# Performance work log

Hardware: AMD Instinct MI355X
Metric: run time of the kernel (lower is better)

Reference implementation:

```python
import jax, jax.numpy as jnp
import numpy as np

BATCH, T, D_MODEL, D_STATE = 32, 4096, 256, 256
RMIN, RMAX, MAX_PHASE = 0.9, 0.999, 6.283
NEG_SLOPE = 0.01  # F.leaky_relu default


def setup_inputs() -> dict:
    key = jax.random.key(0)
    ks = jax.random.split(key, 12)
    x = jax.random.normal(ks[0], (BATCH, T, D_MODEL), jnp.float32)
    done = jnp.zeros((BATCH, T), jnp.bool_)
    h0_re = jnp.zeros((BATCH, D_STATE), jnp.float32)
    h0_im = jnp.zeros((BATCH, D_STATE), jnp.float32)
    # LRU eigenvalue init: |lambda| ~ U[rmin, rmax] (Orvieto et al.)
    u1 = jax.random.uniform(ks[1], (D_STATE,), jnp.float32)
    u2 = jax.random.uniform(ks[2], (D_STATE,), jnp.float32)
    nu_log = jnp.log(-0.5 * jnp.log(u1 * (RMAX**2 - RMIN**2) + RMIN**2))
    theta_log = jnp.log(MAX_PHASE * u2)
    lam_abs = jnp.exp(-jnp.exp(nu_log))
    gamma_log = jnp.log(jnp.sqrt(1.0 - lam_abs**2))
    sB = 1.0 / np.sqrt(2.0 * D_MODEL)
    sC = 1.0 / np.sqrt(D_STATE)
    B_re = jax.random.normal(ks[3], (D_STATE, D_MODEL), jnp.float32) * sB
    B_im = jax.random.normal(ks[4], (D_STATE, D_MODEL), jnp.float32) * sB
    C_re = jax.random.normal(ks[5], (D_STATE, D_STATE), jnp.float32) * sC
    C_im = jax.random.normal(ks[6], (D_STATE, D_STATE), jnp.float32) * sC
    D_mat = jax.random.normal(ks[7], (D_STATE, D_MODEL), jnp.float32) * (1.0 / np.sqrt(D_MODEL))
    mlp_w = jax.random.normal(ks[8], (D_MODEL, D_STATE), jnp.float32) * (1.0 / np.sqrt(D_STATE))
    mlp_b = jnp.zeros((D_MODEL,), jnp.float32)
    ln1_g = jnp.ones((D_MODEL,), jnp.float32); ln1_b = jnp.zeros((D_MODEL,), jnp.float32)
    ln2_g = jnp.ones((D_STATE,), jnp.float32); ln2_b = jnp.zeros((D_STATE,), jnp.float32)
    ln3_g = jnp.ones((D_MODEL,), jnp.float32); ln3_b = jnp.zeros((D_MODEL,), jnp.float32)
    return dict(x=x, done=done, h0_re=h0_re, h0_im=h0_im, nu_log=nu_log,
                theta_log=theta_log, gamma_log=gamma_log, B_re=B_re, B_im=B_im,
                C_re=C_re, C_im=C_im, D_mat=D_mat, mlp_w=mlp_w, mlp_b=mlp_b,
                ln1_g=ln1_g, ln1_b=ln1_b, ln2_g=ln2_g, ln2_b=ln2_b,
                ln3_g=ln3_g, ln3_b=ln3_b)


def _layernorm(x, g, b, eps=1e-5):
    mu = jnp.mean(x, axis=-1, keepdims=True)
    var = jnp.var(x, axis=-1, keepdims=True)
    return (x - mu) * jax.lax.rsqrt(var + eps) * g + b


def _leaky(x):
    return jnp.where(x >= 0, x, NEG_SLOPE * x)


def _forward(x, done, h0_re, h0_im, nu_log, theta_log, gamma_log, B_re, B_im,
             C_re, C_im, D_mat, mlp_w, mlp_b, ln1_g, ln1_b, ln2_g, ln2_b,
             ln3_g, ln3_b):
    z = _layernorm(x, ln1_g, ln1_b)          # [B,T,D]
    skip = z
    z = _leaky(z)
    # diagonal complex recurrence params
    lam_abs = jnp.exp(-jnp.exp(nu_log))
    theta = jnp.exp(theta_log)
    lam_re = lam_abs * jnp.cos(theta)        # [N]
    lam_im = lam_abs * jnp.sin(theta)
    gamma = jnp.exp(gamma_log)
    # input projection: gamma * (B z_t), complex
    u_re = jnp.einsum('btd,nd->btn', z, B_re) * gamma
    u_im = jnp.einsum('btd,nd->btn', z, B_im) * gamma
    mask = 1.0 - done.astype(z.dtype)        # [B,T], reset state where done

    def step(carry, inp):
        hr, hi = carry
        ur, ui, m = inp                       # [B,N],[B,N],[B]
        hr = hr * m[:, None]
        hi = hi * m[:, None]
        nr = lam_re * hr - lam_im * hi + ur
        ni = lam_re * hi + lam_im * hr + ui
        return (nr, ni), (nr, ni)

    xs = (jnp.swapaxes(u_re, 0, 1), jnp.swapaxes(u_im, 0, 1), jnp.swapaxes(mask, 0, 1))
    (_, _), (hs_re, hs_im) = jax.lax.scan(step, (h0_re, h0_im), xs)
    hs_re = jnp.swapaxes(hs_re, 0, 1)         # [B,T,N]
    hs_im = jnp.swapaxes(hs_im, 0, 1)
    # y = Re(C h) + D z
    y = (jnp.einsum('btn,mn->btm', hs_re, C_re)
         - jnp.einsum('btn,mn->btm', hs_im, C_im)
         + jnp.einsum('btd,nd->btn', z, D_mat))
    y = _leaky(_layernorm(y, ln2_g, ln2_b))
    y = jnp.einsum('btn,dn->btd', y, mlp_w) + mlp_b
    y = _layernorm(y, ln3_g, ln3_b)
    return y + skip


def reference(x, done, h0_re, h0_im, nu_log, theta_log, gamma_log, B_re, B_im,
              C_re, C_im, D_mat, mlp_w, mlp_b, ln1_g, ln1_b, ln2_g, ln2_b,
              ln3_g, ln3_b):
    return _forward(x, done, h0_re, h0_im, nu_log, theta_log, gamma_log,
                    B_re, B_im, C_re, C_im, D_mat, mlp_w, mlp_b,
                    ln1_g, ln1_b, ln2_g, ln2_b, ln3_g, ln3_b)
```

## Files before the change

### kernel.cpp

```cpp
#include <hip/hip_runtime.h>

#define BATCH 32
#define TLEN  4096
#define DM    256
#define NS    256
#define BT    (BATCH*TLEN)
#define CHL   64
#define NCH   (TLEN/CHL)

typedef unsigned short u16;
typedef __bf16 bf16x8 __attribute__((ext_vector_type(8)));
typedef float  f32x4  __attribute__((ext_vector_type(4)));

__device__ __forceinline__ u16 f2bf(float f) {
  unsigned u = __builtin_bit_cast(unsigned, f);
  u += 0x7FFFu + ((u >> 16) & 1u);
  return (u16)(u >> 16);
}
__device__ __forceinline__ float bf2f(u16 h) {
  unsigned u = ((unsigned)h) << 16;
  return __builtin_bit_cast(float, u);
}
__device__ __forceinline__ float wsum(float v) {
  #pragma unroll
  for (int m = 32; m >= 1; m >>= 1) v += __shfl_xor(v, m, 64);
  return v;
}
__device__ __forceinline__ void gload_lds16(const void* g, void* l) {
  __builtin_amdgcn_global_load_lds(
      (const __attribute__((address_space(1))) void*)(uintptr_t)g,
      (__attribute__((address_space(3))) void*)(unsigned)(uintptr_t)l,
      16, 0, 0);
}
#define VMCNT(N)  asm volatile("s_waitcnt vmcnt(" #N ")" ::: "memory")
#define LGKM0()   asm volatile("s_waitcnt lgkmcnt(0)" ::: "memory")
#define BARRIER() do { __builtin_amdgcn_s_barrier(); asm volatile("" ::: "memory"); } while (0)

__global__ void k_prep(const float* __restrict__ nu_log, const float* __restrict__ th_log,
                       const float* __restrict__ ga_log,
                       const float* __restrict__ B_re, const float* __restrict__ B_im,
                       const float* __restrict__ C_re, const float* __restrict__ C_im,
                       const float* __restrict__ D_mat, const float* __restrict__ mlp_w,
                       float* __restrict__ lam_re, float* __restrict__ lam_im,
                       u16* __restrict__ WB, u16* __restrict__ W2, u16* __restrict__ WM)
{
  const int tid = blockIdx.x * blockDim.x + threadIdx.x;
  const int nt  = gridDim.x * blockDim.x;
  for (int i = tid; i < NS; i += nt) {
    float la = expf(-expf(nu_log[i]));
    float th = expf(th_log[i]);
    lam_re[i] = la * cosf(th);
    lam_im[i] = la * sinf(th);
  }
  for (int i = tid; i < 512 * DM; i += nt) {
    int n = i >> 8, d = i & 255;
    float v = (n < 256) ? B_re[n * DM + d] * expf(ga_log[n])
                        : B_im[(n - 256) * DM + d] * expf(ga_log[n - 256]);
    WB[i] = f2bf(v);
  }
  for (int i = tid; i < 256 * 768; i += nt) {
    int n = i / 768, k = i - n * 768;
    float v;
    if (k < 256)      v =  C_re[n * 256 + k];
    else if (k < 512) v = -C_im[n * 256 + (k - 256)];
    else              v =  D_mat[n * 256 + (k - 512)];
    W2[i] = f2bf(v);
  }
  for (int i = tid; i < 256 * 256; i += nt) WM[i] = f2bf(mlp_w[i]);
}

__global__ __launch_bounds__(256) void k_ln1(const float* __restrict__ x,
                                             const float* __restrict__ g, const float* __restrict__ b,
                                             u16* __restrict__ za)
{
  const size_t row = (size_t)blockIdx.x * 4 + (threadIdx.x >> 6);
  const int lane = threadIdx.x & 63;
  float4 v = ((const float4*)(x + row * DM))[lane];
  float s = wsum(v.x + v.y + v.z + v.w);
  float q = wsum(v.x * v.x + v.y * v.y + v.z * v.z + v.w * v.w);
  float mean = s * (1.f / DM);
  float rstd = rsqrtf(q * (1.f / DM) - mean * mean + 1e-5f);
  float4 gg = ((const float4*)g)[lane];
  float4 bb = ((const float4*)b)[lane];
  float z0 = (v.x - mean) * rstd * gg.x + bb.x;
  float z1 = (v.y - mean) * rstd * gg.y + bb.y;
  float z2 = (v.z - mean) * rstd * gg.z + bb.z;
  float z3 = (v.w - mean) * rstd * gg.w + bb.w;
  ushort4 zl;
  zl.x = f2bf(z0 >= 0.f ? z0 : 0.01f * z0);
  zl.y = f2bf(z1 >= 0.f ? z1 : 0.01f * z1);
  zl.z = f2bf(z2 >= 0.f ? z2 : 0.01f * z2);
  zl.w = f2bf(z3 >= 0.f ? z3 : 0.01f * z3);
  ((ushort4*)(za + row * DM))[lane] = zl;
}

template <int EPI>
__global__ __launch_bounds__(512, 2) void gemm_fused(
    const u16* __restrict__ A0, int lda0, int ksplit,
    const u16* __restrict__ A1, int lda1,
    int K, const u16* __restrict__ W, int ldw,
    const float* __restrict__ g, const float* __restrict__ b,
    const float* __restrict__ bias, const u16* __restrict__ zsrc,
    u16* __restrict__ outb, float* __restrict__ outf, int ldo)
{
  __shared__ __align__(16) u16 As[2][256 * 64];
  __shared__ __align__(16) u16 Bs[2][256 * 64];
  int mt, nw0;
  if constexpr (EPI == 0) {
    const int bid = blockIdx.x;
    const int xcd = bid & 7, s = bid >> 3;
    mt  = xcd * 64 + (s >> 1);
    nw0 = (s & 1) << 8;
  } else { mt = blockIdx.x; nw0 = 0; }
  const int m0 = mt * 256;
  const int tid = threadIdx.x;
  const int w = tid >> 6, lane = tid & 63;
  const int wr = w >> 1, wc = w & 1;

  f32x4 acc[4][8] = {};

  auto STAGE_A = [&](int p, int k0, int half) {
    const bool second = (k0 >= ksplit);
    const u16* Asrc = second ? A1 : A0;
    const int  alda = second ? lda1 : lda0;
    const int  ak   = second ? (k0 - ksplit) : k0;
    #pragma unroll
    for (int j = 0; j < 2; ++j) {
      const int r = half * 16 + w * 2 + j;
      const int row = r * 8 + (lane >> 3);
      const int col = (((lane & 7) ^ (row & 7)) << 3);
      gload_lds16(Asrc + (size_t)(m0 + row) * alda + ak + col, &As[p][r * 512]);
    }
  };
  auto STAGE_B = [&](int p, int k0, int half) {
    #pragma unroll
    for (int j = 0; j < 2; ++j) {
      const int r = half * 16 + w * 2 + j;
      const int row = r * 8 + (lane >> 3);
      const int col = (((lane & 7) ^ (row & 7)) << 3);
      gload_lds16(W + (size_t)(nw0 + row) * ldw + k0 + col, &Bs[p][r * 512]);
    }
  };

  const int NT = K >> 6;
  STAGE_A(0, 0, 0); STAGE_A(0, 0, 1);
  STAGE_B(0, 0, 0); STAGE_B(0, 0, 1);
  if (NT > 1) { STAGE_A(1, 64, 0); STAGE_A(1, 64, 1); VMCNT(4); }
  else        { VMCNT(0); }
  BARRIER();

  const int lq = (lane >> 4) << 3;

  for (int t = 0; t < NT; ++t) {
    const int p = t & 1;
    const int pn = p ^ 1;
    bf16x8 af[4][2];
    bf16x8 bfr[2][2];

    #pragma unroll
    for (int mi = 0; mi < 4; ++mi) {
      const int ra = wr * 64 + mi * 16 + (lane & 15);
      #pragma unroll
      for (int kki = 0; kki < 2; ++kki) {
        const int koff = kki * 32 + lq;
        af[mi][kki] = *(const bf16x8*)((const char*)&As[p][0] + ra * 128 + ((koff * 2) ^ ((ra & 7) << 4)));
      }
    }
    #pragma unroll
    for (int nn = 0; nn < 2; ++nn) {
      const int rb = wc * 128 + nn * 16 + (lane & 15);
      #pragma unroll
      for (int kki = 0; kki < 2; ++kki) {
        const int koff = kki * 32 + lq;
        bfr[nn][kki] = *(const bf16x8*)((const char*)&Bs[p][0] + rb * 128 + ((koff * 2) ^ ((rb & 7) << 4)));
      }
    }
    if (t + 1 < NT) STAGE_B(pn, (t + 1) << 6, 0);
    BARRIER(); LGKM0();
    __builtin_amdgcn_s_setprio(1);
    #pragma unroll
    for (int kki = 0; kki < 2; ++kki)
      #pragma unroll
      for (int nn = 0; nn < 2; ++nn)
        #pragma unroll
        for (int mi = 0; mi < 4; ++mi)
          acc[mi][nn] = __builtin_amdgcn_mfma_f32_16x16x32_bf16(af[mi][kki], bfr[nn][kki], acc[mi][nn], 0, 0, 0);
    __builtin_amdgcn_s_setprio(0);
    BARRIER();

    #pragma unroll
    for (int q = 1; q < 4; ++q) {
      #pragma unroll
      for (int nn = 0; nn < 2; ++nn) {
        const int rb = wc * 128 + (q * 2 + nn) * 16 + (lane & 15);
        #pragma unroll
        for (int kki = 0; kki < 2; ++kki) {
          const int koff = kki * 32 + lq;
          bfr[nn][kki] = *(const bf16x8*)((const char*)&Bs[p][0] + rb * 128 + ((koff * 2) ^ ((rb & 7) << 4)));
        }
      }
      if (q == 1)      { if (t + 1 < NT) STAGE_B(pn, (t + 1) << 6, 1); }
      else if (q == 2) { if (t + 2 < NT) STAGE_A(p,  (t + 2) << 6, 0); }
      else             { if (t + 2 < NT) STAGE_A(p,  (t + 2) << 6, 1); }
      BARRIER(); LGKM0();
      __builtin_amdgcn_s_setprio(1);
      #pragma unroll
      for (int kki = 0; kki < 2; ++kki)
        #pragma unroll
        for (int nn = 0; nn < 2; ++nn)
          #pragma unroll
          for (int mi = 0; mi < 4; ++mi)
            acc[mi][q * 2 + nn] = __builtin_amdgcn_mfma_f32_16x16x32_bf16(af[mi][kki], bfr[nn][kki], acc[mi][q * 2 + nn], 0, 0, 0);
      __builtin_amdgcn_s_setprio(0);
      if (q == 3) { if (t + 2 < NT) { VMCNT(4); } else { VMCNT(0); } }
      BARRIER();
    }
  }

  const int rq = (lane >> 4) << 2;

  if constexpr (EPI == 0) {
    #pragma unroll
    for (int mi = 0; mi < 4; ++mi) {
      #pragma unroll
      for (int rr = 0; rr < 4; ++rr) {
        const int row = wr * 64 + mi * 16 + rq + rr;
        const size_t rbase = (size_t)(m0 + row) * ldo + nw0;
        #pragma unroll
        for (int ni = 0; ni < 8; ++ni) {
          const int col = wc * 128 + ni * 16 + (lane & 15);
          outb[rbase + col] = f2bf(acc[mi][ni][rr]);
        }
      }
    }
    return;
  }

  float g8[8], b8[8], bias8[8];
  #pragma unroll
  for (int ni = 0; ni < 8; ++ni) {
    const int col = wc * 128 + ni * 16 + (lane & 15);
    g8[ni] = g[col]; b8[ni] = b[col];
    if constexpr (EPI == 2) bias8[ni] = bias[col];
  }

  float* red = (float*)&As[0][0];
  #pragma unroll
  for (int mi = 0; mi < 4; ++mi) {
    #pragma unroll
    for (int rr = 0; rr < 4; ++rr) {
      float s = 0.f, q = 0.f;
      #pragma unroll
      for (int ni = 0; ni < 8; ++ni) {
        float v = acc[mi][ni][rr];
        if constexpr (EPI == 2) v += bias8[ni];
        s += v; q += v * v;
      }
      #pragma unroll
      for (int mm = 1; mm < 16; mm <<= 1) {
        s += __shfl_xor(s, mm, 64);
        q += __shfl_xor(q, mm, 64);
      }
      if ((lane & 15) == 0) {
        const int row = wr * 64 + mi * 16 + rq + rr;
        red[row * 4 + wc * 2]     = s;
        red[row * 4 + wc * 2 + 1] = q;
      }
    }
  }
  __syncthreads();

  #pragma unroll
  for (int mi = 0; mi < 4; ++mi) {
    #pragma unroll
    for (int rr = 0; rr < 4; ++rr) {
      const int row = wr * 64 + mi * 16 + rq + rr;
      const float S = red[row * 4] + red[row * 4 + 2];
      const float Q = red[row * 4 + 1] + red[row * 4 + 3];
      const float mean = S * (1.f / 256.f);
      const float rstd = rsqrtf(Q * (1.f / 256.f) - mean * mean + 1e-5f);
      const size_t rbase = (size_t)(m0 + row) * 256;
      #pragma unroll
      for (int ni = 0; ni < 8; ++ni) {
        const int col = wc * 128 + ni * 16 + (lane & 15);
        float v = acc[mi][ni][rr];
        if constexpr (EPI == 2) v += bias8[ni];
        float t = (v - mean) * rstd * g8[ni] + b8[ni];
        if constexpr (EPI == 1) {
          t = t >= 0.f ? t : 0.01f * t;
          outb[rbase + col] = f2bf(t);
        } else {
          float zv = bf2f(zsrc[rbase + col]);
          zv = zv >= 0.f ? zv : 100.f * zv;
          outf[rbase + col] = t + zv;
        }
      }
    }
  }
}

__global__ __launch_bounds__(256) void scan_passA(const u16* __restrict__ u,
    const unsigned char* __restrict__ done,
    const float* __restrict__ lam_re, const float* __restrict__ lam_im,
    float* __restrict__ Ere, float* __restrict__ Eim,
    float* __restrict__ Are, float* __restrict__ Aim)
{
  const int b = blockIdx.x / NCH, c = blockIdx.x % NCH;
  const int n = threadIdx.x;
  const float lr = lam_re[n], li = lam_im[n];
  float hre = 0.f, him = 0.f, pm = 1.f;
  const int t0 = c * CHL;
  for (int t = t0; t < t0 + CHL; ++t) {
    const float m = done[b * TLEN + t] ? 0.f : 1.f;
    pm *= m;
    const float hr = hre * m, hi = him * m;
    const size_t base = ((size_t)(b * TLEN + t)) * 512;
    const float ur = bf2f(u[base + n]), ui = bf2f(u[base + 256 + n]);
    hre = lr * hr - li * hi + ur;
    him = lr * hi + li * hr + ui;
  }
  const size_t idx = ((size_t)(b * NCH + c)) * NS + n;
  Ere[idx] = hre; Eim[idx] = him;
  float pr = lr, pi = li;
  #pragma unroll
  for (int s = 0; s < 6; ++s) { float a = pr * pr - pi * pi; float bq = 2.f * pr * pi; pr = a; pi = bq; }
  Are[idx] = pr * pm; Aim[idx] = pi * pm;
}

__global__ __launch_bounds__(256) void scan_comb(const float* __restrict__ h0re,
    const float* __restrict__ h0im,
    const float* __restrict__ Are, const float* __restrict__ Aim,
    const float* __restrict__ Ere, const float* __restrict__ Eim,
    float* __restrict__ Sre, float* __restrict__ Sim)
{
  const int b = blockIdx.x, n = threadIdx.x;
  float sre = h0re[b * NS + n], sim = h0im[b * NS + n];
  for (int c = 0; c < NCH; ++c) {
    const size_t idx = ((size_t)(b * NCH + c)) * NS + n;
    Sre[idx] = sre; Sim[idx] = sim;
    const float ar = Are[idx], ai = Aim[idx];
    const float nr = ar * sre - ai * sim + Ere[idx];
    const float ni = ar * sim + ai * sre + Eim[idx];
    sre = nr; sim = ni;
  }
}

__global__ __launch_bounds__(256) void scan_passC(u16* __restrict__ u,
    const unsigned char* __restrict__ done,
    const float* __restrict__ lam_re, const float* __restrict__ lam_im,
    const float* __restrict__ Sre, const float* __restrict__ Sim)
{
  const int b = blockIdx.x / NCH, c = blockIdx.x % NCH;
  const int n = threadIdx.x;
  const float lr = lam_re[n], li = lam_im[n];
  const size_t sidx = ((size_t)(b * NCH + c)) * NS + n;
  float hre = Sre[sidx], him = Sim[sidx];
  const int t0 = c * CHL;
  for (int t = t0; t < t0 + CHL; ++t) {
    const float m = done[b * TLEN + t] ? 0.f : 1.f;
    const float hr = hre * m, hi = him * m;
    const size_t base = ((size_t)(b * TLEN + t)) * 512;
    const float ur = bf2f(u[base + n]), ui = bf2f(u[base + 256 + n]);
    hre = lr * hr - li * hi + ur;
    him = lr * hi + li * hr + ui;
    u[base + n]       = f2bf(hre);
    u[base + 256 + n] = f2bf(him);
  }
}

extern "C" void kernel_launch(void* const* d_in, const int* in_sizes, int n_in,
                              void* d_out, int out_size, void* d_ws, size_t ws_size,
                              hipStream_t stream)
{
  const float* x      = (const float*)d_in[0];
  const unsigned char* done = (const unsigned char*)d_in[1];
  const float* h0re   = (const float*)d_in[2];
  const float* h0im   = (const float*)d_in[3];
  const float* nu_log = (const float*)d_in[4];
  const float* th_log = (const float*)d_in[5];
  const float* ga_log = (const float*)d_in[6];
  const float* B_re   = (const float*)d_in[7];
  const float* B_im   = (const float*)d_in[8];
  const float* C_re   = (const float*)d_in[9];
  const float* C_im   = (const float*)d_in[10];
  const float* D_mat  = (const float*)d_in[11];
  const float* mlp_w  = (const float*)d_in[12];
  const float* mlp_b  = (const float*)d_in[13];
  const float* ln1_g  = (const float*)d_in[14];
  const float* ln1_b  = (const float*)d_in[15];
  const float* ln2_g  = (const float*)d_in[16];
  const float* ln2_b  = (const float*)d_in[17];
  const float* ln3_g  = (const float*)d_in[18];
  const float* ln3_b  = (const float*)d_in[19];
  (void)in_sizes; (void)n_in; (void)out_size; (void)ws_size;

  char* ws = (char*)d_ws;
  float* lam_re = (float*)(ws + 0);
  float* lam_im = (float*)(ws + 1024);
  u16* WB = (u16*)(ws + 4096);
  u16* W2 = (u16*)(ws + 4096 + 512 * 256 * 2);
  u16* WM = (u16*)(ws + 4096 + 512 * 256 * 2 + 256 * 768 * 2);

  size_t off = (size_t)1 << 20;
  u16* za    = (u16*)(ws + off); off += (size_t)BT * DM * 2;
  u16* ubuf  = (u16*)(ws + off); off += (size_t)BT * 512 * 2;
  u16* ybuf  = (u16*)(ws + off); off += (size_t)BT * NS * 2;
  float* Ere = (float*)(ws + off); off += (size_t)BATCH * NCH * NS * 4;
  float* Eim = (float*)(ws + off); off += (size_t)BATCH * NCH * NS * 4;
  float* Are = (float*)(ws + off); off += (size_t)BATCH * NCH * NS * 4;
  float* Aim = (float*)(ws + off); off += (size_t)BATCH * NCH * NS * 4;
  float* Sre = (float*)(ws + off); off += (size_t)BATCH * NCH * NS * 4;
  float* Sim = (float*)(ws + off); off += (size_t)BATCH * NCH * NS * 4;

  k_prep<<<256, 256, 0, stream>>>(nu_log, th_log, ga_log, B_re, B_im, C_re, C_im,
                                  D_mat, mlp_w, lam_re, lam_im, WB, W2, WM);
  k_ln1<<<BT / 4, 256, 0, stream>>>(x, ln1_g, ln1_b, za);
  gemm_fused<0><<<1024, 512, 0, stream>>>(za, 256, 1 << 28, nullptr, 0,
                                          256, WB, 256, nullptr, nullptr,
                                          nullptr, nullptr, ubuf, nullptr, 512);
  scan_passA<<<BATCH * NCH, 256, 0, stream>>>(ubuf, done, lam_re, lam_im, Ere, Eim, Are, Aim);
  scan_comb <<<BATCH,       256, 0, stream>>>(h0re, h0im, Are, Aim, Ere, Eim, Sre, Sim);
  scan_passC<<<BATCH * NCH, 256, 0, stream>>>(ubuf, done, lam_re, lam_im, Sre, Sim);
  gemm_fused<1><<<BT / 256, 512, 0, stream>>>(ubuf, 512, 512, za, 256,
                                              768, W2, 768, ln2_g, ln2_b,
                                              nullptr, nullptr, ybuf, nullptr, 256);
  gemm_fused<2><<<BT / 256, 512, 0, stream>>>(ybuf, 256, 256, ybuf, 256,
                                              256, WM, 256, ln3_g, ln3_b,
                                              mlp_b, za, nullptr, (float*)d_out, 256);
}
```

Measured before the change: 330.5 us.

## Fuse chunk-local scan summary into input-projection GEMM epilogue

Drops the separate scan_passA kernel. The first GEMM epilogue now computes, for each 64-step chunk, the complex decay product and the end state straight from the accumulator registers, using a warp shuffle scan across the row quads. Real and imaginary parts come from separate column halves, so each half writes its own partial E and scan_comb adds the two. This removes one full read of the 256 MB u buffer and one launch, at the cost of a heavier GEMM epilogue and higher register pressure.

New measurement: 367.9 us. 11.3% more time.

```diff
diff --git a/kernel.cpp b/kernel.cpp
--- a/kernel.cpp
+++ b/kernel.cpp
@@ -7,6 +7,7 @@
 #define BT    (BATCH*TLEN)
 #define CHL   64
 #define NCH   (TLEN/CHL)
+#define PSTRIDE ((size_t)BATCH*NCH*NS)
 
 typedef unsigned short u16;
 typedef __bf16 bf16x8 __attribute__((ext_vector_type(8)));
@@ -101,7 +102,11 @@
     int K, const u16* __restrict__ W, int ldw,
     const float* __restrict__ g, const float* __restrict__ b,
     const float* __restrict__ bias, const u16* __restrict__ zsrc,
-    u16* __restrict__ outb, float* __restrict__ outf, int ldo)
+    u16* __restrict__ outb, float* __restrict__ outf, int ldo,
+    const unsigned char* __restrict__ done,
+    const float* __restrict__ lamr, const float* __restrict__ lami,
+    float* __restrict__ Ebase_r, float* __restrict__ Ebase_i,
+    float* __restrict__ Apr, float* __restrict__ Api)
 {
   __shared__ __align__(16) u16 As[2][256 * 64];
   __shared__ __align__(16) u16 Bs[2][256 * 64];
@@ -233,6 +238,64 @@
         }
       }
     }
+    const int hq = lane >> 4;
+    const int ln = lane & 15;
+    const int gchunk = (m0 >> 6) + wr;
+    const int trow0 = m0 + wr * 64;
+    const int part = nw0 >> 8;
+    uchar4 dn[4];
+    #pragma unroll
+    for (int mi = 0; mi < 4; ++mi)
+      dn[mi] = *(const uchar4*)(done + trow0 + mi * 16 + hq * 4);
+    #pragma unroll
+    for (int ni = 0; ni < 8; ++ni) {
+      const int n = wc * 128 + ni * 16 + ln;
+      const float lr = lamr[n], li = lami[n];
+      float Ar = 1.f, Ai = 0.f, Er = 0.f, Ei = 0.f;
+      #pragma unroll
+      for (int mi = 0; mi < 4; ++mi) {
+        float ar = 1.f, ai = 0.f, er = 0.f, ei = 0.f;
+        #pragma unroll
+        for (int rr = 0; rr < 4; ++rr) {
+          const unsigned char db = (rr == 0) ? dn[mi].x : (rr == 1) ? dn[mi].y
+                                 : (rr == 2) ? dn[mi].z : dn[mi].w;
+          const float m = db ? 0.f : 1.f;
+          const float uv = acc[mi][ni][rr];
+          const float ur = part == 0 ? uv : 0.f;
+          const float ui = part == 0 ? 0.f : uv;
+          const float lmr = lr * m, lmi = li * m;
+          const float na_r = lmr * ar - lmi * ai, na_i = lmr * ai + lmi * ar;
+          ar = na_r; ai = na_i;
+          const float ne_r = lmr * er - lmi * ei + ur;
+          const float ne_i = lmr * ei + lmi * er + ui;
+          er = ne_r; ei = ne_i;
+        }
+        #pragma unroll
+        for (int d = 1; d <= 2; d <<= 1) {
+          int sl = lane - 16 * d; sl = sl < 0 ? lane : sl;
+          const float pa_r = __shfl(ar, sl, 64), pa_i = __shfl(ai, sl, 64);
+          const float pe_r = __shfl(er, sl, 64), pe_i = __shfl(ei, sl, 64);
+          if (hq >= d) {
+            const float ca_r = ar * pa_r - ai * pa_i, ca_i = ar * pa_i + ai * pa_r;
+            const float ce_r = er + (ar * pe_r - ai * pe_i);
+            const float ce_i = ei + (ar * pe_i + ai * pe_r);
+            ar = ca_r; ai = ca_i; er = ce_r; ei = ce_i;
+          }
+        }
+        ar = __shfl(ar, ln + 48, 64); ai = __shfl(ai, ln + 48, 64);
+        er = __shfl(er, ln + 48, 64); ei = __shfl(ei, ln + 48, 64);
+        const float nA_r = ar * Ar - ai * Ai, nA_i = ar * Ai + ai * Ar;
+        const float nE_r = er + (ar * Er - ai * Ei);
+        const float nE_i = ei + (ar * Ei + ai * Er);
+        Ar = nA_r; Ai = nA_i; Er = nE_r; Ei = nE_i;
+      }
+      if (hq == 0) {
+        const size_t idx = (size_t)gchunk * 256 + n;
+        Ebase_r[(size_t)part * PSTRIDE + idx] = Er;
+        Ebase_i[(size_t)part * PSTRIDE + idx] = Ei;
+        if (part == 0) { Apr[idx] = Ar; Api[idx] = Ai; }
+      }
+    }
     return;
   }
 
@@ -299,38 +362,10 @@
   }
 }
 
-__global__ __launch_bounds__(256) void scan_passA(const u16* __restrict__ u,
-    const unsigned char* __restrict__ done,
-    const float* __restrict__ lam_re, const float* __restrict__ lam_im,
-    float* __restrict__ Ere, float* __restrict__ Eim,
-    float* __restrict__ Are, float* __restrict__ Aim)
-{
-  const int b = blockIdx.x / NCH, c = blockIdx.x % NCH;
-  const int n = threadIdx.x;
-  const float lr = lam_re[n], li = lam_im[n];
-  float hre = 0.f, him = 0.f, pm = 1.f;
-  const int t0 = c * CHL;
-  for (int t = t0; t < t0 + CHL; ++t) {
-    const float m = done[b * TLEN + t] ? 0.f : 1.f;
-    pm *= m;
-    const float hr = hre * m, hi = him * m;
-    const size_t base = ((size_t)(b * TLEN + t)) * 512;
-    const float ur = bf2f(u[base + n]), ui = bf2f(u[base + 256 + n]);
-    hre = lr * hr - li * hi + ur;
-    him = lr * hi + li * hr + ui;
-  }
-  const size_t idx = ((size_t)(b * NCH + c)) * NS + n;
-  Ere[idx] = hre; Eim[idx] = him;
-  float pr = lr, pi = li;
-  #pragma unroll
-  for (int s = 0; s < 6; ++s) { float a = pr * pr - pi * pi; float bq = 2.f * pr * pi; pr = a; pi = bq; }
-  Are[idx] = pr * pm; Aim[idx] = pi * pm;
-}
-
 __global__ __launch_bounds__(256) void scan_comb(const float* __restrict__ h0re,
     const float* __restrict__ h0im,
-    const float* __restrict__ Are, const float* __restrict__ Aim,
-    const float* __restrict__ Ere, const float* __restrict__ Eim,
+    const float* __restrict__ Apr, const float* __restrict__ Api,
+    const float* __restrict__ Er, const float* __restrict__ Ei,
     float* __restrict__ Sre, float* __restrict__ Sim)
 {
   const int b = blockIdx.x, n = threadIdx.x;
@@ -338,9 +373,11 @@
   for (int c = 0; c < NCH; ++c) {
     const size_t idx = ((size_t)(b * NCH + c)) * NS + n;
     Sre[idx] = sre; Sim[idx] = sim;
-    const float ar = Are[idx], ai = Aim[idx];
-    const float nr = ar * sre - ai * sim + Ere[idx];
-    const float ni = ar * sim + ai * sre + Eim[idx];
+    const float ar = Apr[idx], ai = Api[idx];
+    const float er = Er[idx] + Er[PSTRIDE + idx];
+    const float ei = Ei[idx] + Ei[PSTRIDE + idx];
+    const float nr = ar * sre - ai * sim + er;
+    const float ni = ar * sim + ai * sre + ei;
     sre = nr; sim = ni;
   }
 }
@@ -405,26 +442,30 @@
   u16* za    = (u16*)(ws + off); off += (size_t)BT * DM * 2;
   u16* ubuf  = (u16*)(ws + off); off += (size_t)BT * 512 * 2;
   u16* ybuf  = (u16*)(ws + off); off += (size_t)BT * NS * 2;
-  float* Ere = (float*)(ws + off); off += (size_t)BATCH * NCH * NS * 4;
-  float* Eim = (float*)(ws + off); off += (size_t)BATCH * NCH * NS * 4;
-  float* Are = (float*)(ws + off); off += (size_t)BATCH * NCH * NS * 4;
-  float* Aim = (float*)(ws + off); off += (size_t)BATCH * NCH * NS * 4;
-  float* Sre = (float*)(ws + off); off += (size_t)BATCH * NCH * NS * 4;
-  float* Sim = (float*)(ws + off); off += (size_t)BATCH * NCH * NS * 4;
+  float* Apr = (float*)(ws + off); off += PSTRIDE * 4;
+  float* Api = (float*)(ws + off); off += PSTRIDE * 4;
+  float* Er  = (float*)(ws + off); off += PSTRIDE * 4 * 2;
+  float* Ei  = (float*)(ws + off); off += PSTRIDE * 4 * 2;
+  float* Sre = (float*)(ws + off); off += PSTRIDE * 4;
+  float* Sim = (float*)(ws + off); off += PSTRIDE * 4;
 
   k_prep<<<256, 256, 0, stream>>>(nu_log, th_log, ga_log, B_re, B_im, C_re, C_im,
                                   D_mat, mlp_w, lam_re, lam_im, WB, W2, WM);
   k_ln1<<<BT / 4, 256, 0, stream>>>(x, ln1_g, ln1_b, za);
   gemm_fused<0><<<1024, 512, 0, stream>>>(za, 256, 1 << 28, nullptr, 0,
                                           256, WB, 256, nullptr, nullptr,
-                                          nullptr, nullptr, ubuf, nullptr, 512);
-  scan_passA<<<BATCH * NCH, 256, 0, stream>>>(ubuf, done, lam_re, lam_im, Ere, Eim, Are, Aim);
-  scan_comb <<<BATCH,       256, 0, stream>>>(h0re, h0im, Are, Aim, Ere, Eim, Sre, Sim);
+                                          nullptr, nullptr, ubuf, nullptr, 512,
+                                          done, lam_re, lam_im, Er, Ei, Apr, Api);
+  scan_comb<<<BATCH, 256, 0, stream>>>(h0re, h0im, Apr, Api, Er, Ei, Sre, Sim);
   scan_passC<<<BATCH * NCH, 256, 0, stream>>>(ubuf, done, lam_re, lam_im, Sre, Sim);
   gemm_fused<1><<<BT / 256, 512, 0, stream>>>(ubuf, 512, 512, za, 256,
                                               768, W2, 768, ln2_g, ln2_b,
-                                              nullptr, nullptr, ybuf, nullptr, 256);
+                                              nullptr, nullptr, ybuf, nullptr, 256,
+                                              nullptr, nullptr, nullptr,
+                                              nullptr, nullptr, nullptr, nullptr);
   gemm_fused<2><<<BT / 256, 512, 0, stream>>>(ybuf, 256, 256, ybuf, 256,
                                               256, WM, 256, ln3_g, ln3_b,
-                                              mlp_b, za, nullptr, (float*)d_out, 256);
-}
+                                              mlp_b, za, nullptr, (float*)d_out, 256,
+                                              nullptr, nullptr, nullptr,
+                                              nullptr, nullptr, nullptr, nullptr);
+}
```

## Split GEMM kernel into specialized u-projection and smaller-tile LayerNorm GEMMs

Applied to the files above, without the earlier changes.

The templated GEMM is split in two. One kernel keeps the 256x256 tile for the input projection, with its strides and trip count hard-coded. The two LayerNorm-epilogue GEMMs use a new kernel with 128-row M tiles, K steps of 32, a new LDS swizzle and launch bounds raised to 4 blocks per CU. This doubles the grid (1024 blocks) so occupancy and latency hiding improve. In exchange, the full 256-column B tile is reloaded twice as often per output row and there are more barriers per K.

Measured after the change: 346.0 us. +4.7%, slower.

```diff
diff --git a/kernel.cpp b/kernel.cpp
--- a/kernel.cpp
+++ b/kernel.cpp
@@ -94,24 +94,16 @@
   ((ushort4*)(za + row * DM))[lane] = zl;
 }
 
-template <int EPI>
-__global__ __launch_bounds__(512, 2) void gemm_fused(
-    const u16* __restrict__ A0, int lda0, int ksplit,
-    const u16* __restrict__ A1, int lda1,
-    int K, const u16* __restrict__ W, int ldw,
-    const float* __restrict__ g, const float* __restrict__ b,
-    const float* __restrict__ bias, const u16* __restrict__ zsrc,
-    u16* __restrict__ outb, float* __restrict__ outf, int ldo)
+__global__ __launch_bounds__(512, 2) void gemm_u4(
+    const u16* __restrict__ A0, const u16* __restrict__ W,
+    u16* __restrict__ outb)
 {
   __shared__ __align__(16) u16 As[2][256 * 64];
   __shared__ __align__(16) u16 Bs[2][256 * 64];
-  int mt, nw0;
-  if constexpr (EPI == 0) {
-    const int bid = blockIdx.x;
-    const int xcd = bid & 7, s = bid >> 3;
-    mt  = xcd * 64 + (s >> 1);
-    nw0 = (s & 1) << 8;
-  } else { mt = blockIdx.x; nw0 = 0; }
+  const int bid = blockIdx.x;
+  const int xcd = bid & 7, sl = bid >> 3;
+  const int mt  = xcd * 64 + (sl >> 1);
+  const int nw0 = (sl & 1) << 8;
   const int m0 = mt * 256;
   const int tid = threadIdx.x;
   const int w = tid >> 6, lane = tid & 63;
@@ -120,16 +112,12 @@
   f32x4 acc[4][8] = {};
 
   auto STAGE_A = [&](int p, int k0, int half) {
-    const bool second = (k0 >= ksplit);
-    const u16* Asrc = second ? A1 : A0;
-    const int  alda = second ? lda1 : lda0;
-    const int  ak   = second ? (k0 - ksplit) : k0;
     #pragma unroll
     for (int j = 0; j < 2; ++j) {
       const int r = half * 16 + w * 2 + j;
       const int row = r * 8 + (lane >> 3);
       const int col = (((lane & 7) ^ (row & 7)) << 3);
-      gload_lds16(Asrc + (size_t)(m0 + row) * alda + ak + col, &As[p][r * 512]);
+      gload_lds16(A0 + (size_t)(m0 + row) * 256 + k0 + col, &As[p][r * 512]);
     }
   };
   auto STAGE_B = [&](int p, int k0, int half) {
@@ -138,15 +126,14 @@
       const int r = half * 16 + w * 2 + j;
       const int row = r * 8 + (lane >> 3);
       const int col = (((lane & 7) ^ (row & 7)) << 3);
-      gload_lds16(W + (size_t)(nw0 + row) * ldw + k0 + col, &Bs[p][r * 512]);
+      gload_lds16(W + (size_t)(nw0 + row) * 256 + k0 + col, &Bs[p][r * 512]);
     }
   };
 
-  const int NT = K >> 6;
+  const int NT = 4;
   STAGE_A(0, 0, 0); STAGE_A(0, 0, 1);
   STAGE_B(0, 0, 0); STAGE_B(0, 0, 1);
-  if (NT > 1) { STAGE_A(1, 64, 0); STAGE_A(1, 64, 1); VMCNT(4); }
-  else        { VMCNT(0); }
+  STAGE_A(1, 64, 0); STAGE_A(1, 64, 1); VMCNT(4);
   BARRIER();
 
   const int lq = (lane >> 4) << 3;
@@ -218,35 +205,119 @@
   }
 
   const int rq = (lane >> 4) << 2;
-
-  if constexpr (EPI == 0) {
-    #pragma unroll
-    for (int mi = 0; mi < 4; ++mi) {
-      #pragma unroll
-      for (int rr = 0; rr < 4; ++rr) {
-        const int row = wr * 64 + mi * 16 + rq + rr;
-        const size_t rbase = (size_t)(m0 + row) * ldo + nw0;
-        #pragma unroll
-        for (int ni = 0; ni < 8; ++ni) {
-          const int col = wc * 128 + ni * 16 + (lane & 15);
-          outb[rbase + col] = f2bf(acc[mi][ni][rr]);
-        }
-      }
-    }
-    return;
-  }
-
+  #pragma unroll
+  for (int mi = 0; mi < 4; ++mi) {
+    #pragma unroll
+    for (int rr = 0; rr < 4; ++rr) {
+      const int row = wr * 64 + mi * 16 + rq + rr;
+      const size_t rbase = (size_t)(m0 + row) * 512 + nw0;
+      #pragma unroll
+      for (int ni = 0; ni < 8; ++ni) {
+        const int col = wc * 128 + ni * 16 + (lane & 15);
+        outb[rbase + col] = f2bf(acc[mi][ni][rr]);
+      }
+    }
+  }
+}
+
+template <int EPI>
+__global__ __launch_bounds__(512, 4) void gemm_ln(
+    const u16* __restrict__ A0, int lda0, int ksplit,
+    const u16* __restrict__ A1, int lda1,
+    int K, const u16* __restrict__ W, int ldw,
+    const float* __restrict__ g, const float* __restrict__ b,
+    const float* __restrict__ bias, const u16* __restrict__ zsrc,
+    u16* __restrict__ outb, float* __restrict__ outf)
+{
+  __shared__ __align__(16) u16 As[2][128 * 32];
+  __shared__ __align__(16) u16 Bs[2][256 * 32];
+  const int m0 = blockIdx.x * 128;
+  const int tid = threadIdx.x;
+  const int w = tid >> 6, lane = tid & 63;
+  const int wr = w >> 1, wc = w & 1;
+  const int ln = lane & 15;
+  const int kg = lane >> 4;
+
+  f32x4 acc[2][8] = {};
+
+  auto STAGE_A = [&](int p, int k0) {
+    const bool second = (k0 >= ksplit);
+    const u16* Asrc = second ? A1 : A0;
+    const int  alda = second ? lda1 : lda0;
+    const int  ak   = second ? (k0 - ksplit) : k0;
+    const int row = tid >> 2;
+    const int sch = (tid & 3) ^ ((row >> 1) & 3);
+    gload_lds16(Asrc + (size_t)(m0 + row) * alda + ak + (sch << 3), &As[p][tid * 8]);
+  };
+  auto STAGE_B = [&](int p, int k0, int half) {
+    const int idx2 = half * 512 + tid;
+    const int row = idx2 >> 2;
+    const int sch = (idx2 & 3) ^ ((row >> 1) & 3);
+    gload_lds16(W + (size_t)row * ldw + k0 + (sch << 3), &Bs[p][idx2 * 8]);
+  };
+
+  const int NT = K >> 5;
+  STAGE_A(0, 0); STAGE_B(0, 0, 0); STAGE_B(0, 0, 1);
+  STAGE_A(1, 32);
+  VMCNT(1);
+  BARRIER();
+
+  for (int t = 0; t < NT; ++t) {
+    const int p = t & 1, pn = p ^ 1;
+    bf16x8 af[2], bfr[4];
+
+    #pragma unroll
+    for (int mi = 0; mi < 2; ++mi) {
+      const int ra = wr * 32 + mi * 16 + ln;
+      af[mi] = *(const bf16x8*)((const char*)&As[p][0] + ra * 64 + ((kg ^ ((ra >> 1) & 3)) << 4));
+    }
+    #pragma unroll
+    for (int j = 0; j < 4; ++j) {
+      const int rb = wc * 128 + j * 16 + ln;
+      bfr[j] = *(const bf16x8*)((const char*)&Bs[p][0] + rb * 64 + ((kg ^ ((rb >> 1) & 3)) << 4));
+    }
+    if (t + 1 < NT) STAGE_B(pn, (t + 1) << 5, 0);
+    BARRIER(); LGKM0();
+    __builtin_amdgcn_s_setprio(1);
+    #pragma unroll
+    for (int j = 0; j < 4; ++j)
+      #pragma unroll
+      for (int mi = 0; mi < 2; ++mi)
+        acc[mi][j] = __builtin_amdgcn_mfma_f32_16x16x32_bf16(af[mi], bfr[j], acc[mi][j], 0, 0, 0);
+    __builtin_amdgcn_s_setprio(0);
+    BARRIER();
+
+    #pragma unroll
+    for (int j = 0; j < 4; ++j) {
+      const int rb = wc * 128 + (4 + j) * 16 + ln;
+      bfr[j] = *(const bf16x8*)((const char*)&Bs[p][0] + rb * 64 + ((kg ^ ((rb >> 1) & 3)) << 4));
+    }
+    if (t + 1 < NT) STAGE_B(pn, (t + 1) << 5, 1);
+    if (t + 2 < NT) STAGE_A(p, (t + 2) << 5);
+    BARRIER(); LGKM0();
+    __builtin_amdgcn_s_setprio(1);
+    #pragma unroll
+    for (int j = 0; j < 4; ++j)
+      #pragma unroll
+      for (int mi = 0; mi < 2; ++mi)
+        acc[mi][4 + j] = __builtin_amdgcn_mfma_f32_16x16x32_bf16(af[mi], bfr[j], acc[mi][4 + j], 0, 0, 0);
+    __builtin_amdgcn_s_setprio(0);
+    if (t + 2 < NT) { VMCNT(1); } else { VMCNT(0); }
+    BARRIER();
+  }
+
+  const int rq = (lane >> 4) << 2;
   float g8[8], b8[8], bias8[8];
   #pragma unroll
   for (int ni = 0; ni < 8; ++ni) {
-    const int col = wc * 128 + ni * 16 + (lane & 15);
+    const int col = wc * 128 + ni * 16 + ln;
     g8[ni] = g[col]; b8[ni] = b[col];
     if constexpr (EPI == 2) bias8[ni] = bias[col];
   }
 
   float* red = (float*)&As[0][0];
   #pragma unroll
-  for (int mi = 0; mi < 4; ++mi) {
+  for (int mi = 0; mi < 2; ++mi) {
     #pragma unroll
     for (int rr = 0; rr < 4; ++rr) {
       float s = 0.f, q = 0.f;
@@ -261,8 +332,8 @@
         s += __shfl_xor(s, mm, 64);
         q += __shfl_xor(q, mm, 64);
       }
-      if ((lane & 15) == 0) {
-        const int row = wr * 64 + mi * 16 + rq + rr;
+      if (ln == 0) {
+        const int row = wr * 32 + mi * 16 + rq + rr;
         red[row * 4 + wc * 2]     = s;
         red[row * 4 + wc * 2 + 1] = q;
       }
@@ -271,10 +342,10 @@
   __syncthreads();
 
   #pragma unroll
-  for (int mi = 0; mi < 4; ++mi) {
+  for (int mi = 0; mi < 2; ++mi) {
     #pragma unroll
     for (int rr = 0; rr < 4; ++rr) {
-      const int row = wr * 64 + mi * 16 + rq + rr;
+      const int row = wr * 32 + mi * 16 + rq + rr;
       const float S = red[row * 4] + red[row * 4 + 2];
       const float Q = red[row * 4 + 1] + red[row * 4 + 3];
       const float mean = S * (1.f / 256.f);
@@ -282,7 +353,7 @@
       const size_t rbase = (size_t)(m0 + row) * 256;
       #pragma unroll
       for (int ni = 0; ni < 8; ++ni) {
-        const int col = wc * 128 + ni * 16 + (lane & 15);
+        const int col = wc * 128 + ni * 16 + ln;
         float v = acc[mi][ni][rr];
         if constexpr (EPI == 2) v += bias8[ni];
         float t = (v - mean) * rstd * g8[ni] + b8[ni];
@@ -415,16 +486,14 @@
   k_prep<<<256, 256, 0, stream>>>(nu_log, th_log, ga_log, B_re, B_im, C_re, C_im,
                                   D_mat, mlp_w, lam_re, lam_im, WB, W2, WM);
   k_ln1<<<BT / 4, 256, 0, stream>>>(x, ln1_g, ln1_b, za);
-  gemm_fused<0><<<1024, 512, 0, stream>>>(za, 256, 1 << 28, nullptr, 0,
-                                          256, WB, 256, nullptr, nullptr,
-                                          nullptr, nullptr, ubuf, nullptr, 512);
+  gemm_u4<<<1024, 512, 0, stream>>>(za, WB, ubuf);
   scan_passA<<<BATCH * NCH, 256, 0, stream>>>(ubuf, done, lam_re, lam_im, Ere, Eim, Are, Aim);
   scan_comb <<<BATCH,       256, 0, stream>>>(h0re, h0im, Are, Aim, Ere, Eim, Sre, Sim);
   scan_passC<<<BATCH * NCH, 256, 0, stream>>>(ubuf, done, lam_re, lam_im, Sre, Sim);
-  gemm_fused<1><<<BT / 256, 512, 0, stream>>>(ubuf, 512, 512, za, 256,
-                                              768, W2, 768, ln2_g, ln2_b,
-                                              nullptr, nullptr, ybuf, nullptr, 256);
-  gemm_fused<2><<<BT / 256, 512, 0, stream>>>(ybuf, 256, 256, ybuf, 256,
-                                              256, WM, 256, ln3_g, ln3_b,
-                                              mlp_b, za, nullptr, (float*)d_out, 256);
-}
+  gemm_ln<1><<<BT / 128, 512, 0, stream>>>(ubuf, 512, 512, za, 256,
+                                           768, W2, 768, ln2_g, ln2_b,
+                                           nullptr, nullptr, ybuf, nullptr);
+  gemm_ln<2><<<BT / 128, 512, 0, stream>>>(ybuf, 256, 1 << 28, nullptr, 0,
+                                           256, WM, 256, ln3_g, ln3_b,
+                                           mlp_b, za, nullptr, (float*)d_out);
+}
```
